# Kernel optimization log

Measured on AMD Instinct MI355X. Metric: run time of the kernel, lower is better.

The kernel has to match this reference:

```python
import jax, jax.numpy as jnp
import numpy as np

N = 768      # n_proto (number of class prototypes)
D = 128      # trans_feat_num
H = D // 16  # edge-MLP hidden = 8
A = 312      # semantic attribute dim
INIT_TEMP = 0.1
VTEMP = 10.0
STEMP = 10.0
EPS = 1e-8


def _layer_norm(x, g, b, eps=1e-5):
    m = x.mean(-1, keepdims=True)
    v = ((x - m) ** 2).mean(-1, keepdims=True)
    return (x - m) / jnp.sqrt(v + eps) * g + b


def _instance_norm_rows(x, eps=1e-5):
    # torch InstanceNorm1d on 2D input: unbatched (C, L) -> normalize each row, no affine
    m = x.mean(-1, keepdims=True)
    v = ((x - m) ** 2).mean(-1, keepdims=True)
    return (x - m) / jnp.sqrt(v + eps)


def _init_edge(x, temp):
    # pairwise cosine similarity + row softmax
    nrm = jnp.linalg.norm(x, axis=1)
    sim = (x @ x.T) / jnp.maximum(nrm[:, None] * nrm[None, :], EPS)
    return jax.nn.softmax(sim / temp, axis=-1)


def _edge_update(proto, last_edge, W1, b1, W2, b2, temp):
    n, d = proto.shape
    # O(n^2) pairwise squared differences  -> [n*n, d]
    feat = ((proto[:, None, :] - proto[None, :, :]) ** 2).reshape(n * n, d)
    h = jax.nn.relu(_instance_norm_rows(feat @ W1.T + b1))  # [n*n, H]
    e = jnp.tanh(h @ W2.T + b2).reshape(n, n)
    return jax.nn.softmax(e * (last_edge + EPS) / temp, axis=-1)


def _node_update(proto, last_edge, edge, W, b, g, beta):
    extra = last_edge @ proto          # cross-modal message (dist_injection)
    p = edge @ proto                   # same-modal aggregation
    return jax.nn.relu(_layer_norm((p + extra) @ W.T + b, g, beta)) + p


def setup_inputs() -> dict:
    key = jax.random.key(0)
    ks = jax.random.split(key, 9)
    rn = lambda k, shape, s=1.0: jax.random.normal(k, shape, dtype=jnp.float32) * s
    return {
        "visual_proto": rn(ks[0], (N, D)),
        "semantic_proto": rn(ks[1], (N, D)),
        "attribute": rn(ks[2], (N, A)),
        "Wvn": rn(ks[3], (D, D), 0.08), "bvn": jnp.zeros((D,), jnp.float32),
        "gvn": jnp.ones((D,), jnp.float32), "betavn": jnp.zeros((D,), jnp.float32),
        "Wve1": rn(ks[4], (H, D), 0.1), "bve1": jnp.zeros((H,), jnp.float32),
        "Wve2": rn(ks[5], (1, H), 0.3), "bve2": jnp.zeros((1,), jnp.float32),
        "Wsn": rn(ks[6], (D, D), 0.08), "bsn": jnp.zeros((D,), jnp.float32),
        "gsn": jnp.ones((D,), jnp.float32), "betasn": jnp.zeros((D,), jnp.float32),
        "Wse1": rn(ks[7], (H, D), 0.1), "bse1": jnp.zeros((H,), jnp.float32),
        "Wse2": rn(ks[8], (1, H), 0.3), "bse2": jnp.zeros((1,), jnp.float32),
    }


def reference(visual_proto, semantic_proto, attribute,
              Wvn, bvn, gvn, betavn, Wve1, bve1, Wve2, bve2,
              Wsn, bsn, gsn, betasn, Wse1, bse1, Wse2, bse2):
    ve = _init_edge(visual_proto, INIT_TEMP)
    se = _init_edge(attribute, INIT_TEMP)
    vp = _node_update(visual_proto, se, ve, Wvn, bvn, gvn, betavn)
    ve2 = _edge_update(vp, ve, Wve1, bve1, Wve2, bve2, VTEMP)
    sp = _node_update(semantic_proto, ve2, se, Wsn, bsn, gsn, betasn)
    se2 = _edge_update(sp, se, Wse1, bse1, Wse2, bse2, STEMP)
    return vp, sp, ve2, se2
```

## Files before the change

### kernel.cpp

```cpp
#include <hip/hip_runtime.h>
#include <math.h>

#define NN 768
#define DD 128
#define AA 312
#define HH 8
#define CEPS 1e-8f

typedef __attribute__((ext_vector_type(8))) short s8b;
typedef __attribute__((ext_vector_type(4))) float f4v;

__device__ __forceinline__ float wave_sum(float v) {
    #pragma unroll
    for (int o = 32; o; o >>= 1) v += __shfl_down(v, o, 64);
    return v;
}
__device__ __forceinline__ float wave_max(float v) {
    #pragma unroll
    for (int o = 32; o; o >>= 1) v = fmaxf(v, __shfl_down(v, o, 64));
    return v;
}
__device__ __forceinline__ unsigned short f2bf(float f) {
    unsigned u = __float_as_uint(f);
    u += 0x7FFFu + ((u >> 16) & 1u);
    return (unsigned short)(u >> 16);
}

template <int COLS>
__device__ void gram_tile(const float* __restrict__ A, float invtemp, float* __restrict__ sim,
                          int i0, int j0, int tid, float* As, float* Bs) {
    const int tx = tid & 15, ty = tid >> 4;
    const int lr = tid >> 3, lc4 = (tid & 7) * 4;
    float acc00 = 0.f, acc01 = 0.f, acc10 = 0.f, acc11 = 0.f;
    float si0 = 0.f, si1 = 0.f, sj0 = 0.f, sj1 = 0.f;
    for (int kc = 0; kc < COLS; kc += 32) {
        float4 av, bv;
        if (kc + lc4 + 4 <= COLS) {
            av = *(const float4*)(A + (size_t)(i0 + lr) * COLS + kc + lc4);
            bv = *(const float4*)(A + (size_t)(j0 + lr) * COLS + kc + lc4);
        } else {
            float ta[4], tb[4];
            #pragma unroll
            for (int l = 0; l < 4; ++l) {
                int c = kc + lc4 + l;
                ta[l] = (c < COLS) ? A[(size_t)(i0 + lr) * COLS + c] : 0.f;
                tb[l] = (c < COLS) ? A[(size_t)(j0 + lr) * COLS + c] : 0.f;
            }
            av = make_float4(ta[0], ta[1], ta[2], ta[3]);
            bv = make_float4(tb[0], tb[1], tb[2], tb[3]);
        }
        __syncthreads();
        As[(lc4 + 0) * 34 + lr] = av.x; As[(lc4 + 1) * 34 + lr] = av.y;
        As[(lc4 + 2) * 34 + lr] = av.z; As[(lc4 + 3) * 34 + lr] = av.w;
        Bs[(lc4 + 0) * 34 + lr] = bv.x; Bs[(lc4 + 1) * 34 + lr] = bv.y;
        Bs[(lc4 + 2) * 34 + lr] = bv.z; Bs[(lc4 + 3) * 34 + lr] = bv.w;
        __syncthreads();
        #pragma unroll
        for (int k = 0; k < 32; ++k) {
            float2 aa = *(const float2*)&As[k * 34 + 2 * ty];
            float2 bb = *(const float2*)&Bs[k * 34 + 2 * tx];
            acc00 = fmaf(aa.x, bb.x, acc00);
            acc01 = fmaf(aa.x, bb.y, acc01);
            acc10 = fmaf(aa.y, bb.x, acc10);
            acc11 = fmaf(aa.y, bb.y, acc11);
            si0 = fmaf(aa.x, aa.x, si0);
            si1 = fmaf(aa.y, aa.y, si1);
            sj0 = fmaf(bb.x, bb.x, sj0);
            sj1 = fmaf(bb.y, bb.y, sj1);
        }
    }
    const float ni0 = sqrtf(si0), ni1 = sqrtf(si1);
    const float nj0 = sqrtf(sj0), nj1 = sqrtf(sj1);
    float* s0 = sim + (size_t)(i0 + 2 * ty) * NN + j0 + 2 * tx;
    float* s1 = s0 + NN;
    s0[0] = acc00 / fmaxf(ni0 * nj0, CEPS) * invtemp;
    s0[1] = acc01 / fmaxf(ni0 * nj1, CEPS) * invtemp;
    s1[0] = acc10 / fmaxf(ni1 * nj0, CEPS) * invtemp;
    s1[1] = acc11 / fmaxf(ni1 * nj1, CEPS) * invtemp;
}

__global__ __launch_bounds__(256) void gram_prep_kernel(
    const float* __restrict__ visual, const float* __restrict__ attribute,
    const float* __restrict__ Wvn, const float* __restrict__ Wsn, float* __restrict__ simv,
    float* __restrict__ sima, float* __restrict__ WvnT, float* __restrict__ WsnT) {
    __shared__ __align__(16) float smem[2176];
    const int tid = threadIdx.x;
    const int task = blockIdx.x;
    if (task < 576) {
        gram_tile<DD>(visual, 10.f, simv, (task / 24) * 32, (task % 24) * 32, tid, smem,
                      smem + 1088);
    } else if (task < 1152) {
        const int rem = task - 576;
        gram_tile<AA>(attribute, 10.f, sima, (rem / 24) * 32, (rem % 24) * 32, tid, smem,
                      smem + 1088);
    } else {
        const int u = task - 1152;
        const float* S = (u >= 16) ? Wsn : Wvn;
        float* Dt = (u >= 16) ? WsnT : WvnT;
        const int tile = u & 15;
        const int c0 = (tile & 3) * 32, r0 = (tile >> 2) * 32;
        const int tx = tid & 31, ty = tid >> 5;
        #pragma unroll
        for (int rr = ty; rr < 32; rr += 8)
            smem[rr * 33 + tx] = S[(size_t)(r0 + rr) * DD + c0 + tx];
        __syncthreads();
        #pragma unroll
        for (int rr = ty; rr < 32; rr += 8)
            Dt[(size_t)(c0 + rr) * DD + r0 + tx] = smem[tx * 33 + rr];
    }
}

__device__ void softmax_row_g(const float* __restrict__ vr, float* __restrict__ dst, int tid,
                              float* red) {
    float v0 = vr[tid], v1 = vr[tid + 256], v2 = vr[tid + 512];
    float m = wave_max(fmaxf(fmaxf(v0, v1), v2));
    if ((tid & 63) == 0) red[tid >> 6] = m;
    __syncthreads();
    m = fmaxf(fmaxf(red[0], red[1]), fmaxf(red[2], red[3]));
    float e0 = __expf(v0 - m), e1 = __expf(v1 - m), e2 = __expf(v2 - m);
    float sw = wave_sum(e0 + e1 + e2);
    if ((tid & 63) == 0) red[4 + (tid >> 6)] = sw;
    __syncthreads();
    const float s = red[4] + red[5] + red[6] + red[7];
    const float inv = 1.f / s;
    dst[tid] = e0 * inv;
    dst[tid + 256] = e1 * inv;
    dst[tid + 512] = e2 * inv;
}

__global__ __launch_bounds__(256) void softmax_all_kernel(const float* __restrict__ simv,
                                                          const float* __restrict__ sima,
                                                          float* __restrict__ ve,
                                                          float* __restrict__ se) {
    __shared__ float red[8];
    const int task = blockIdx.x;
    const float* src = (task < NN) ? simv + (size_t)task * NN : sima + (size_t)(task - NN) * NN;
    float* dst = (task < NN) ? ve + (size_t)task * NN : se + (size_t)(task - NN) * NN;
    softmax_row_g(src, dst, threadIdx.x, red);
}

__global__ __launch_bounds__(256) void softmax_out_kernel(const float* __restrict__ L,
                                                          float* __restrict__ dst) {
    __shared__ float red[8];
    const int i = blockIdx.x;
    softmax_row_g(L + (size_t)i * NN, dst + (size_t)i * NN, threadIdx.x, red);
}

__device__ void block_softmax768(float* buf, int tid, float* red) {
    const int w = tid >> 6, lane = tid & 63;
    float v0 = buf[tid];
    float v1 = (tid < NN - 512) ? buf[tid + 512] : -3.4e38f;
    float m = wave_max(fmaxf(v0, v1));
    if (lane == 0) red[w] = m;
    __syncthreads();
    m = red[0];
    #pragma unroll
    for (int i = 1; i < 8; ++i) m = fmaxf(m, red[i]);
    float e0 = __expf(v0 - m);
    float e1 = (tid < NN - 512) ? __expf(v1 - m) : 0.f;
    float sw = wave_sum(e0 + e1);
    if (lane == 0) red[8 + w] = sw;
    __syncthreads();
    float s = 0.f;
    #pragma unroll
    for (int i = 0; i < 8; ++i) s += red[8 + i];
    const float inv = 1.f / s;
    buf[tid] = e0 * inv;
    if (tid < NN - 512) buf[tid + 512] = e1 * inv;
    __syncthreads();
}

template <bool EXSM>
__global__ __launch_bounds__(512) void node_kernel(
    const float* __restrict__ P, const float* __restrict__ Ep, const float* __restrict__ ExOrL,
    const float* __restrict__ WT, const float* __restrict__ b, const float* __restrict__ g,
    const float* __restrict__ beta, float* __restrict__ out, const float* __restrict__ W1e,
    short* __restrict__ outb, float* __restrict__ cvec, float* __restrict__ exOut) {
    __shared__ __align__(16) float ep[2][NN], ex[2][NN];
    __shared__ __align__(16) float pp[4][2][DD], xx[4][2][DD];
    __shared__ __align__(16) float qs[2][DD], tps[2][2][DD];
    __shared__ float red[16];
    const int i0 = blockIdx.x * 2;
    const int tid = threadIdx.x;
    const int s = (tid >> 7) & 3, d = tid & 127;
    #pragma unroll
    for (int r = 0; r < 2; ++r)
        for (int k = tid; k < NN; k += 512) {
            ep[r][k] = Ep[(size_t)(i0 + r) * NN + k];
            ex[r][k] = ExOrL[(size_t)(i0 + r) * NN + k];
        }
    __syncthreads();
    if (EXSM) {
        block_softmax768(ex[0], tid, red);
        block_softmax768(ex[1], tid, red);
        #pragma unroll
        for (int r = 0; r < 2; ++r)
            for (int k = tid; k < NN; k += 512) exOut[(size_t)(i0 + r) * NN + k] = ex[r][k];
    }
    float p0 = 0.f, x0 = 0.f, p1 = 0.f, x1 = 0.f;
    const int kb = s * 192;
    #pragma unroll 4
    for (int kk = 0; kk < 192; ++kk) {
        const int k = kb + kk;
        const float pv = P[(size_t)k * DD + d];
        p0 = fmaf(ep[0][k], pv, p0);
        x0 = fmaf(ex[0][k], pv, x0);
        p1 = fmaf(ep[1][k], pv, p1);
        x1 = fmaf(ex[1][k], pv, x1);
    }
    pp[s][0][d] = p0; xx[s][0][d] = x0;
    pp[s][1][d] = p1; xx[s][1][d] = x1;
    __syncthreads();
    const int rr = (tid >> 7) & 1;
    float preg = 0.f;
    if (tid < 256) {
        float p = pp[0][rr][d] + pp[1][rr][d] + pp[2][rr][d] + pp[3][rr][d];
        float x = xx[0][rr][d] + xx[1][rr][d] + xx[2][rr][d] + xx[3][rr][d];
        qs[rr][d] = p + x;
        preg = p;
    }
    __syncthreads();
    {
        const int sc = tid >> 8, rr2 = (tid >> 7) & 1;
        float t = (sc == 0) ? b[d] : 0.f;
        const int c0 = sc * 64;
        #pragma unroll 4
        for (int c = c0; c < c0 + 64; ++c) t = fmaf(qs[rr2][c], WT[(size_t)c * DD + d], t);
        tps[sc][rr2][d] = t;
    }
    __syncthreads();
    float tval = 0.f;
    if (tid < 256) tval = tps[0][rr][d] + tps[1][rr][d];
    float sm = wave_sum(tid < 256 ? tval : 0.f);
    if ((tid & 63) == 0) red[tid >> 6] = sm;
    __syncthreads();
    if (tid < 256) tval -= (red[2 * rr] + red[2 * rr + 1]) * (1.f / DD);
    float s2 = wave_sum(tid < 256 ? tval * tval : 0.f);
    if ((tid & 63) == 0) red[8 + (tid >> 6)] = s2;
    __syncthreads();
    if (tid < 256) {
        const float var = (red[8 + 2 * rr] + red[8 + 2 * rr + 1]) * (1.f / DD);
        const float ln = tval * rsqrtf(var + 1e-5f) * g[d] + beta[d];
        const float val = fmaxf(ln, 0.f) + preg;
        out[(size_t)(i0 + rr) * DD + d] = val;
        outb[(size_t)(i0 + rr) * DD + d] = (short)f2bf(val);
        qs[rr][d] = val;
    }
    __syncthreads();
    if (tid < 16) {
        const int row = tid >> 3, r = tid & 7;
        float ssum = 0.f;
        for (int k = 0; k < DD; ++k) {
            const float pv = qs[row][k];
            ssum = fmaf(W1e[r * DD + k], pv * pv, ssum);
        }
        cvec[(size_t)(i0 + row) * HH + r] = ssum;
    }
}

__global__ __launch_bounds__(256) void edge_gemm_kernel(
    const float* __restrict__ PR, const short* __restrict__ PRb, const float* __restrict__ cvec,
    const float* __restrict__ Elast, const float* __restrict__ W1, const float* __restrict__ b1,
    const float* __restrict__ W2, const float* __restrict__ b2, float invtemp,
    float* __restrict__ Lout) {
    const int bp = blockIdx.x / 3;
    const int i0 = bp * 2;
    const int jbase = (blockIdx.x % 3) * 256;
    const int tid = threadIdx.x;
    const int lane = tid & 63, wave = tid >> 6;
    __shared__ __align__(16) float pi[2][DD];
    __shared__ __align__(16) float w1s[HH * DD];
    __shared__ __align__(16) short a_sw[4 * 64 * 8];
    if (tid < 256) pi[tid >> 7][tid & 127] = PR[(size_t)(i0 + (tid >> 7)) * DD + (tid & 127)];
    ((float4*)w1s)[tid] = ((const float4*)W1)[tid];
    __syncthreads();
    {
        const int t = tid >> 6, m = lane & 15, q = lane >> 4;
        const int il = m >> 3, r = m & 7;
        const int kb = t * 32 + q * 8;
        s8b av;
        #pragma unroll
        for (int e = 0; e < 8; ++e)
            av[e] = (short)f2bf(pi[il][kb + e] * w1s[r * DD + kb + e]);
        *(s8b*)&a_sw[(t * 64 + lane) * 8] = av;
    }
    __syncthreads();
    s8b af[4];
    #pragma unroll
    for (int t = 0; t < 4; ++t) af[t] = *(const s8b*)&a_sw[(t * 64 + lane) * 8];
    const int q = lane >> 4, n = lane & 15;
    const int rbase = (q & 1) * 4;
    const int il = q >> 1;
    const float4 ci4 = *(const float4*)&cvec[(size_t)(i0 + il) * HH + rbase];
    const float4 b14 = *(const float4*)&b1[rbase];
    const float4 w24 = *(const float4*)&W2[rbase];
    const float b2s = b2[0];
    #pragma unroll
    for (int s = 0; s < 4; ++s) {
        const int j = jbase + (wave * 4 + s) * 16 + n;
        f4v acc = {0.f, 0.f, 0.f, 0.f};
        #pragma unroll
        for (int t = 0; t < 4; ++t) {
            const s8b bf = *(const s8b*)(PRb + (size_t)j * DD + t * 32 + q * 8);
            acc = __builtin_amdgcn_mfma_f32_16x16x32_bf16(af[t], bf, acc, 0, 0, 0);
        }
        const float4 cj = *(const float4*)&cvec[(size_t)j * HH + rbase];
        float z[4];
        z[0] = ci4.x + cj.x - 2.f * acc[0] + b14.x;
        z[1] = ci4.y + cj.y - 2.f * acc[1] + b14.y;
        z[2] = ci4.z + cj.z - 2.f * acc[2] + b14.z;
        z[3] = ci4.w + cj.w - 2.f * acc[3] + b14.w;
        float s1 = z[0] + z[1] + z[2] + z[3];
        float s2 = z[0] * z[0] + z[1] * z[1] + z[2] * z[2] + z[3] * z[3];
        s1 += __shfl_xor(s1, 16, 64);
        s2 += __shfl_xor(s2, 16, 64);
        const float mean = s1 * (1.f / HH);
        const float var = fmaxf(s2 * (1.f / HH) - mean * mean, 0.f);
        const float istd = rsqrtf(var + 1e-5f);
        float a2 = 0.f;
        a2 = fmaf(fmaxf((z[0] - mean) * istd, 0.f), w24.x, a2);
        a2 = fmaf(fmaxf((z[1] - mean) * istd, 0.f), w24.y, a2);
        a2 = fmaf(fmaxf((z[2] - mean) * istd, 0.f), w24.z, a2);
        a2 = fmaf(fmaxf((z[3] - mean) * istd, 0.f), w24.w, a2);
        a2 += __shfl_xor(a2, 16, 64);
        const float tv = tanhf(a2 + b2s);
        const float lv = Elast[(size_t)(i0 + il) * NN + j];
        if ((q & 1) == 0) Lout[(size_t)(i0 + il) * NN + j] = tv * (lv + CEPS) * invtemp;
    }
}

extern "C" void kernel_launch(void* const* d_in, const int* in_sizes, int n_in, void* d_out,
                              int out_size, void* d_ws, size_t ws_size, hipStream_t stream) {
    const float* visual    = (const float*)d_in[0];
    const float* semantic  = (const float*)d_in[1];
    const float* attribute = (const float*)d_in[2];
    const float* Wvn  = (const float*)d_in[3];
    const float* bvn  = (const float*)d_in[4];
    const float* gvn  = (const float*)d_in[5];
    const float* betavn = (const float*)d_in[6];
    const float* Wve1 = (const float*)d_in[7];
    const float* bve1 = (const float*)d_in[8];
    const float* Wve2 = (const float*)d_in[9];
    const float* bve2 = (const float*)d_in[10];
    const float* Wsn  = (const float*)d_in[11];
    const float* bsn  = (const float*)d_in[12];
    const float* gsn  = (const float*)d_in[13];
    const float* betasn = (const float*)d_in[14];
    const float* Wse1 = (const float*)d_in[15];
    const float* bse1 = (const float*)d_in[16];
    const float* Wse2 = (const float*)d_in[17];
    const float* bse2 = (const float*)d_in[18];

    float* out = (float*)d_out;
    float* vp  = out;
    float* sp  = out + 98304;
    float* ve2 = out + 196608;
    float* se2 = out + 786432;

    float* ws    = (float*)d_ws;
    float* simv  = ws;
    float* sima  = ws + 589824;
    float* ve    = ws + 1179648;
    float* se    = ws + 1769472;
    float* L     = ws + 2359296;
    float* WvnT  = ws + 2949120;
    float* WsnT  = ws + 2965504;
    float* cvec1 = ws + 2981888;
    float* cvec2 = ws + 2988032;
    short* vpb   = (short*)(ws + 2994176);
    short* spb   = (short*)(ws + 3043328);

    gram_prep_kernel<<<1184, 256, 0, stream>>>(visual, attribute, Wvn, Wsn, simv, sima, WvnT,
                                               WsnT);
    softmax_all_kernel<<<1536, 256, 0, stream>>>(simv, sima, ve, se);
    node_kernel<false><<<NN / 2, 512, 0, stream>>>(visual, ve, se, WvnT, bvn, gvn, betavn, vp,
                                                   Wve1, vpb, cvec1, nullptr);
    edge_gemm_kernel<<<(NN / 2) * 3, 256, 0, stream>>>(vp, vpb, cvec1, ve, Wve1, bve1, Wve2,
                                                       bve2, 0.1f, L);
    node_kernel<true><<<NN / 2, 512, 0, stream>>>(semantic, se, L, WsnT, bsn, gsn, betasn, sp,
                                                  Wse1, spb, cvec2, ve2);
    edge_gemm_kernel<<<(NN / 2) * 3, 256, 0, stream>>>(sp, spb, cvec2, se, Wse1, bse1, Wse2,
                                                       bse2, 0.1f, L);
    softmax_out_kernel<<<NN, 256, 0, stream>>>(L, se2);
}
```

Measured before the change: 196.8 us.

## Fuse row softmax into edge kernel and parallelize cvec reduction

The edge kernel now handles two full rows per 512-thread block. It writes the logits to shared memory and runs the row softmax in place, so the separate softmax kernel and the softmax inside node_kernel are gone, along with the L round-trip through global memory. The cvec computation in node_kernel now runs on 256 threads with a shuffle reduction instead of 16 serial threads. The trade-off is fewer blocks for the edge stage (384 instead of 1152), which may lower occupancy and latency hiding.

```diff
diff --git a/kernel.cpp b/kernel.cpp
--- a/kernel.cpp
+++ b/kernel.cpp
@@ -139,13 +139,6 @@
     softmax_row_g(src, dst, threadIdx.x, red);
 }
 
-__global__ __launch_bounds__(256) void softmax_out_kernel(const float* __restrict__ L,
-                                                          float* __restrict__ dst) {
-    __shared__ float red[8];
-    const int i = blockIdx.x;
-    softmax_row_g(L + (size_t)i * NN, dst + (size_t)i * NN, threadIdx.x, red);
-}
-
 __device__ void block_softmax768(float* buf, int tid, float* red) {
     const int w = tid >> 6, lane = tid & 63;
     float v0 = buf[tid];
@@ -170,12 +163,11 @@
     __syncthreads();
 }
 
-template <bool EXSM>
 __global__ __launch_bounds__(512) void node_kernel(
-    const float* __restrict__ P, const float* __restrict__ Ep, const float* __restrict__ ExOrL,
+    const float* __restrict__ P, const float* __restrict__ Ep, const float* __restrict__ Ex,
     const float* __restrict__ WT, const float* __restrict__ b, const float* __restrict__ g,
     const float* __restrict__ beta, float* __restrict__ out, const float* __restrict__ W1e,
-    short* __restrict__ outb, float* __restrict__ cvec, float* __restrict__ exOut) {
+    short* __restrict__ outb, float* __restrict__ cvec) {
     __shared__ __align__(16) float ep[2][NN], ex[2][NN];
     __shared__ __align__(16) float pp[4][2][DD], xx[4][2][DD];
     __shared__ __align__(16) float qs[2][DD], tps[2][2][DD];
@@ -187,16 +179,9 @@
     for (int r = 0; r < 2; ++r)
         for (int k = tid; k < NN; k += 512) {
             ep[r][k] = Ep[(size_t)(i0 + r) * NN + k];
-            ex[r][k] = ExOrL[(size_t)(i0 + r) * NN + k];
-        }
-    __syncthreads();
-    if (EXSM) {
-        block_softmax768(ex[0], tid, red);
-        block_softmax768(ex[1], tid, red);
-        #pragma unroll
-        for (int r = 0; r < 2; ++r)
-            for (int k = tid; k < NN; k += 512) exOut[(size_t)(i0 + r) * NN + k] = ex[r][k];
-    }
+            ex[r][k] = Ex[(size_t)(i0 + r) * NN + k];
+        }
+    __syncthreads();
     float p0 = 0.f, x0 = 0.f, p1 = 0.f, x1 = 0.f;
     const int kb = s * 192;
     #pragma unroll 4
@@ -247,37 +232,43 @@
         qs[rr][d] = val;
     }
     __syncthreads();
-    if (tid < 16) {
-        const int row = tid >> 3, r = tid & 7;
+    if (tid < 256) {
+        const int row = tid >> 7, r = (tid >> 4) & 7, l16 = tid & 15;
         float ssum = 0.f;
-        for (int k = 0; k < DD; ++k) {
+        #pragma unroll
+        for (int t = 0; t < 8; ++t) {
+            const int k = l16 + 16 * t;
             const float pv = qs[row][k];
             ssum = fmaf(W1e[r * DD + k], pv * pv, ssum);
         }
-        cvec[(size_t)(i0 + row) * HH + r] = ssum;
-    }
-}
-
-__global__ __launch_bounds__(256) void edge_gemm_kernel(
+        #pragma unroll
+        for (int o = 8; o; o >>= 1) ssum += __shfl_down(ssum, o, 16);
+        if (l16 == 0) cvec[(size_t)(i0 + row) * HH + r] = ssum;
+    }
+}
+
+__global__ __launch_bounds__(512) void edge_fused_kernel(
     const float* __restrict__ PR, const short* __restrict__ PRb, const float* __restrict__ cvec,
     const float* __restrict__ Elast, const float* __restrict__ W1, const float* __restrict__ b1,
     const float* __restrict__ W2, const float* __restrict__ b2, float invtemp,
-    float* __restrict__ Lout) {
-    const int bp = blockIdx.x / 3;
-    const int i0 = bp * 2;
-    const int jbase = (blockIdx.x % 3) * 256;
+    float* __restrict__ out) {
+    const int i0 = blockIdx.x * 2;
     const int tid = threadIdx.x;
     const int lane = tid & 63, wave = tid >> 6;
     __shared__ __align__(16) float pi[2][DD];
     __shared__ __align__(16) float w1s[HH * DD];
     __shared__ __align__(16) short a_sw[4 * 64 * 8];
-    if (tid < 256) pi[tid >> 7][tid & 127] = PR[(size_t)(i0 + (tid >> 7)) * DD + (tid & 127)];
-    ((float4*)w1s)[tid] = ((const float4*)W1)[tid];
-    __syncthreads();
-    {
-        const int t = tid >> 6, m = lane & 15, q = lane >> 4;
+    __shared__ __align__(16) float Ls[2][NN];
+    __shared__ float red[16];
+    if (tid < 256) {
+        pi[tid >> 7][tid & 127] = PR[(size_t)(i0 + (tid >> 7)) * DD + (tid & 127)];
+        ((float4*)w1s)[tid] = ((const float4*)W1)[tid];
+    }
+    __syncthreads();
+    if (tid < 256) {
+        const int t = tid >> 6, m = lane & 15, q2 = lane >> 4;
         const int il = m >> 3, r = m & 7;
-        const int kb = t * 32 + q * 8;
+        const int kb = t * 32 + q2 * 8;
         s8b av;
         #pragma unroll
         for (int e = 0; e < 8; ++e)
@@ -296,8 +287,8 @@
     const float4 w24 = *(const float4*)&W2[rbase];
     const float b2s = b2[0];
     #pragma unroll
-    for (int s = 0; s < 4; ++s) {
-        const int j = jbase + (wave * 4 + s) * 16 + n;
+    for (int s = 0; s < 6; ++s) {
+        const int j = wave * 96 + s * 16 + n;
         f4v acc = {0.f, 0.f, 0.f, 0.f};
         #pragma unroll
         for (int t = 0; t < 4; ++t) {
@@ -325,7 +316,18 @@
         a2 += __shfl_xor(a2, 16, 64);
         const float tv = tanhf(a2 + b2s);
         const float lv = Elast[(size_t)(i0 + il) * NN + j];
-        if ((q & 1) == 0) Lout[(size_t)(i0 + il) * NN + j] = tv * (lv + CEPS) * invtemp;
+        if ((q & 1) == 0) Ls[il][j] = tv * (lv + CEPS) * invtemp;
+    }
+    __syncthreads();
+    block_softmax768(Ls[0], tid, red);
+    block_softmax768(Ls[1], tid, red);
+    float* d0 = out + (size_t)i0 * NN;
+    float* d1 = out + (size_t)(i0 + 1) * NN;
+    d0[tid] = Ls[0][tid];
+    d1[tid] = Ls[1][tid];
+    if (tid < NN - 512) {
+        d0[tid + 512] = Ls[0][tid + 512];
+        d1[tid + 512] = Ls[1][tid + 512];
     }
 }
 
@@ -362,7 +364,6 @@
     float* sima  = ws + 589824;
     float* ve    = ws + 1179648;
     float* se    = ws + 1769472;
-    float* L     = ws + 2359296;
     float* WvnT  = ws + 2949120;
     float* WsnT  = ws + 2965504;
     float* cvec1 = ws + 2981888;
@@ -373,13 +374,12 @@
     gram_prep_kernel<<<1184, 256, 0, stream>>>(visual, attribute, Wvn, Wsn, simv, sima, WvnT,
                                                WsnT);
     softmax_all_kernel<<<1536, 256, 0, stream>>>(simv, sima, ve, se);
-    node_kernel<false><<<NN / 2, 512, 0, stream>>>(visual, ve, se, WvnT, bvn, gvn, betavn, vp,
-                                                   Wve1, vpb, cvec1, nullptr);
-    edge_gemm_kernel<<<(NN / 2) * 3, 256, 0, stream>>>(vp, vpb, cvec1, ve, Wve1, bve1, Wve2,
-                                                       bve2, 0.1f, L);
-    node_kernel<true><<<NN / 2, 512, 0, stream>>>(semantic, se, L, WsnT, bsn, gsn, betasn, sp,
-                                                  Wse1, spb, cvec2, ve2);
-    edge_gemm_kernel<<<(NN / 2) * 3, 256, 0, stream>>>(sp, spb, cvec2, se, Wse1, bse1, Wse2,
-                                                       bse2, 0.1f, L);
-    softmax_out_kernel<<<NN, 256, 0, stream>>>(L, se2);
-}
+    node_kernel<<<NN / 2, 512, 0, stream>>>(visual, ve, se, WvnT, bvn, gvn, betavn, vp, Wve1,
+                                            vpb, cvec1);
+    edge_fused_kernel<<<NN / 2, 512, 0, stream>>>(vp, vpb, cvec1, ve, Wve1, bve1, Wve2, bve2,
+                                                  0.1f, ve2);
+    node_kernel<<<NN / 2, 512, 0, stream>>>(semantic, se, ve2, WsnT, bsn, gsn, betasn, sp, Wse1,
+                                            spb, cvec2);
+    edge_fused_kernel<<<NN / 2, 512, 0, stream>>>(sp, spb, cvec2, se, Wse1, bse1, Wse2, bse2,
+                                                  0.1f, se2);
+}
```

After: 194.5 us. Within noise of the previous version (-1.1%).
